# Kernel optimization log

Measured on AMD Instinct MI355X. Metric: run time of the kernel, lower is better.

Reference implementation:

```python
import jax, jax.numpy as jnp
import numpy as np

EMB = 512
N_ROWS = 10000
N_PAIRS = 65536


def setup_inputs() -> dict:
    key = jax.random.key(0)
    ks = jax.random.split(key, 10)
    s1 = 1.0 / np.sqrt(2 * EMB)
    s2 = 1.0 / np.sqrt(128)
    s3 = 1.0 / np.sqrt(64)
    return {
        "pos_pairs": jax.random.randint(ks[0], (N_PAIRS, 3), 0, N_ROWS, dtype=jnp.int32),
        "neg_pairs": jax.random.randint(ks[1], (N_PAIRS, 3), 0, N_ROWS, dtype=jnp.int32),
        "drug_embedding": jax.random.normal(ks[2], (N_ROWS, EMB), dtype=jnp.float32),
        "target_embedding": jax.random.normal(ks[3], (N_ROWS, EMB), dtype=jnp.float32),
        "W1": jax.random.normal(ks[4], (2 * EMB, 128), dtype=jnp.float32) * s1,
        "b1": jnp.zeros((128,), dtype=jnp.float32),
        "W2": jax.random.normal(ks[5], (128, 64), dtype=jnp.float32) * s2,
        "b2": jnp.zeros((64,), dtype=jnp.float32),
        "W3": jax.random.normal(ks[6], (64, 1), dtype=jnp.float32) * s3,
        "b3": jnp.zeros((1,), dtype=jnp.float32),
    }


def _mlp(x, W1, b1, W2, b2, W3, b3):
    h = jax.nn.relu(x @ W1 + b1)
    h = jax.nn.relu(h @ W2 + b2)
    return (h @ W3 + b3)[..., 0]  # [N]


def _pair_loss(pairs, drug_emb, tgt_emb, W1, b1, W2, b2, W3, b3):
    d = drug_emb[pairs[:, 0]]            # [N, EMB]
    t1 = tgt_emb[pairs[:, 1]]            # [N, EMB]
    t2 = tgt_emb[pairs[:, 2]]            # [N, EMB]
    a1 = _mlp(jnp.concatenate([d, t1], axis=-1), W1, b1, W2, b2, W3, b3)
    a2 = _mlp(jnp.concatenate([d, t2], axis=-1), W1, b1, W2, b2, W3, b3)
    # per-pair MSE of scalar affinities = (a1 - a2)^2; mean over pairs
    return jnp.mean((a1 - a2) ** 2)


def reference(pos_pairs, neg_pairs, drug_embedding, target_embedding,
              W1, b1, W2, b2, W3, b3):
    pos = _pair_loss(pos_pairs, drug_embedding, target_embedding, W1, b1, W2, b2, W3, b3)
    neg = _pair_loss(neg_pairs, drug_embedding, target_embedding, W1, b1, W2, b2, W3, b3)
    return pos - neg
```

## Files before the change

kernel.cpp:

```cpp
#include <hip/hip_runtime.h>

#define EMB 512
#define NROWS 10000
#define NPAIRS 65536

typedef __bf16 bf16x8 __attribute__((ext_vector_type(8)));
typedef float  f32x4  __attribute__((ext_vector_type(4)));
typedef unsigned int u32x4 __attribute__((ext_vector_type(4)));

__device__ __forceinline__ void split2(float x0, float x1, unsigned* hw, unsigned* lw) {
    unsigned u0 = __float_as_uint(x0), u1 = __float_as_uint(x1);
    unsigned r0 = u0 + 0x7FFFu + ((u0 >> 16) & 1u);
    unsigned r1 = u1 + 0x7FFFu + ((u1 >> 16) & 1u);
    float h0 = __uint_as_float(r0 & 0xFFFF0000u);
    float h1 = __uint_as_float(r1 & 0xFFFF0000u);
    float l0 = x0 - h0, l1 = x1 - h1;
    unsigned v0 = __float_as_uint(l0), v1 = __float_as_uint(l1);
    unsigned s0 = v0 + 0x7FFFu + ((v0 >> 16) & 1u);
    unsigned s1 = v1 + 0x7FFFu + ((v1 >> 16) & 1u);
    *hw = (r0 >> 16) | (r1 & 0xFFFF0000u);
    *lw = (s0 >> 16) | (s1 & 0xFFFF0000u);
}

__global__ __launch_bounds__(256)
void k0_fragment(const float* __restrict__ W1, const float* __restrict__ W2,
                 unsigned short* __restrict__ W1Fhi, unsigned short* __restrict__ W1Flo,
                 unsigned short* __restrict__ W2Fhi, unsigned short* __restrict__ W2Flo)
{
    int e = blockIdx.x * 256 + threadIdx.x;
    float x;
    unsigned short *hp, *lp;
    if (e < 131072) {
        int i  = e & 7;
        int l  = (e >> 3) & 63;
        int nt = (e >> 9) & 7;
        int kt = (e >> 12) & 15;
        int t  = e >> 16;
        int k = kt * 32 + 8 * (l >> 4) + i;
        int n = nt * 16 + (l & 15);
        x = W1[(t * 512 + k) * 128 + n];
        hp = W1Fhi + e; lp = W1Flo + e;
    } else {
        int e2 = e - 131072;
        int i  = e2 & 7;
        int l  = (e2 >> 3) & 63;
        int nt = (e2 >> 9) & 3;
        int kt = e2 >> 11;
        int k = kt * 32 + 8 * (l >> 4) + i;
        int n = nt * 16 + (l & 15);
        x = W2[k * 64 + n];
        hp = W2Fhi + e2; lp = W2Flo + e2;
    }
    unsigned u = __float_as_uint(x);
    unsigned r = u + 0x7FFFu + ((u >> 16) & 1u);
    float hf = __uint_as_float(r & 0xFFFF0000u);
    float lf = x - hf;
    unsigned v = __float_as_uint(lf);
    unsigned s = v + 0x7FFFu + ((v >> 16) & 1u);
    *hp = (unsigned short)(r >> 16);
    *lp = (unsigned short)(s >> 16);
}

#define K1_TILES 625

__global__ __launch_bounds__(256)
void k1_mfma(const float* __restrict__ drug, const float* __restrict__ tgt,
             const unsigned* __restrict__ W1Fhi, const unsigned* __restrict__ W1Flo,
             const float* __restrict__ b1,
             float* __restrict__ D, float* __restrict__ T)
{
    int bid = blockIdx.x, tid = threadIdx.x;
    bool isT = bid >= K1_TILES;
    int rt = isT ? bid - K1_TILES : bid;
    const float* emb = isT ? tgt : drug;
    float* out = isT ? T : D;
    int row0 = rt * 16;

    int wave = tid >> 6, lane = tid & 63;
    int g = lane >> 4, lm = lane & 15;
    int ntb = wave * 2;

    const u32x4* BH = (const u32x4*)W1Fhi + (isT ? 8192 : 0);
    const u32x4* BL = (const u32x4*)W1Flo + (isT ? 8192 : 0);

    const float* abase = emb + (size_t)(row0 + lm) * EMB + 8 * g;

    f32x4 acc[2];
    #pragma unroll
    for (int j = 0; j < 2; j++) { acc[j][0]=0.f; acc[j][1]=0.f; acc[j][2]=0.f; acc[j][3]=0.f; }

    float4 a0c = *(const float4*)(abase);
    float4 a1c = *(const float4*)(abase + 4);
    u32x4 bh0c = BH[ntb * 64 + lane];
    u32x4 bh1c = BH[(ntb + 1) * 64 + lane];
    u32x4 bl0c = BL[ntb * 64 + lane];
    u32x4 bl1c = BL[(ntb + 1) * 64 + lane];
    __builtin_amdgcn_sched_barrier(0);

    #pragma unroll
    for (int kt = 0; kt < 16; kt++) {
        float4 a0n, a1n;
        u32x4 bh0n, bh1n, bl0n, bl1n;
        if (kt < 15) {
            a0n = *(const float4*)(abase + (kt + 1) * 32);
            a1n = *(const float4*)(abase + (kt + 1) * 32 + 4);
            bh0n = BH[((kt + 1) * 8 + ntb) * 64 + lane];
            bh1n = BH[((kt + 1) * 8 + ntb + 1) * 64 + lane];
            bl0n = BL[((kt + 1) * 8 + ntb) * 64 + lane];
            bl1n = BL[((kt + 1) * 8 + ntb + 1) * 64 + lane];
        }
        __builtin_amdgcn_sched_barrier(0);
        unsigned h0, h1, h2, h3, l0, l1, l2, l3;
        split2(a0c.x, a0c.y, &h0, &l0);
        split2(a0c.z, a0c.w, &h1, &l1);
        split2(a1c.x, a1c.y, &h2, &l2);
        split2(a1c.z, a1c.w, &h3, &l3);
        u32x4 ah, al;
        ah[0]=h0; ah[1]=h1; ah[2]=h2; ah[3]=h3;
        al[0]=l0; al[1]=l1; al[2]=l2; al[3]=l3;
        bf16x8 Ah = __builtin_bit_cast(bf16x8, ah);
        bf16x8 Al = __builtin_bit_cast(bf16x8, al);
        bf16x8 Bh0 = __builtin_bit_cast(bf16x8, bh0c);
        bf16x8 Bh1 = __builtin_bit_cast(bf16x8, bh1c);
        bf16x8 Bl0 = __builtin_bit_cast(bf16x8, bl0c);
        bf16x8 Bl1 = __builtin_bit_cast(bf16x8, bl1c);
        acc[0] = __builtin_amdgcn_mfma_f32_16x16x32_bf16(Ah, Bh0, acc[0], 0, 0, 0);
        acc[1] = __builtin_amdgcn_mfma_f32_16x16x32_bf16(Ah, Bh1, acc[1], 0, 0, 0);
        acc[0] = __builtin_amdgcn_mfma_f32_16x16x32_bf16(Ah, Bl0, acc[0], 0, 0, 0);
        acc[1] = __builtin_amdgcn_mfma_f32_16x16x32_bf16(Ah, Bl1, acc[1], 0, 0, 0);
        acc[0] = __builtin_amdgcn_mfma_f32_16x16x32_bf16(Al, Bh0, acc[0], 0, 0, 0);
        acc[1] = __builtin_amdgcn_mfma_f32_16x16x32_bf16(Al, Bh1, acc[1], 0, 0, 0);
        __builtin_amdgcn_sched_barrier(0);
        a0c = a0n; a1c = a1n;
        bh0c = bh0n; bh1c = bh1n; bl0c = bl0n; bl1c = bl1n;
    }

    #pragma unroll
    for (int j = 0; j < 2; j++) {
        int col = (ntb + j) * 16 + lm;
        float bias = isT ? 0.f : b1[col];
        #pragma unroll
        for (int reg = 0; reg < 4; reg++) {
            int row = row0 + 4 * g + reg;
            out[row * 128 + col] = acc[j][reg] + bias;
        }
    }
}

__global__ __launch_bounds__(256)
void k2_pairs(const float* __restrict__ D, const float* __restrict__ T,
              const int* __restrict__ pos, const int* __restrict__ neg,
              const unsigned* __restrict__ W2Fhi, const unsigned* __restrict__ W2Flo,
              const float* __restrict__ b2, const float* __restrict__ W3,
              double* __restrict__ partials)
{
    __shared__ u32x4 Ash[4][768];

    int tid = threadIdx.x;
    int wave = tid >> 6, lane = tid & 63;
    int g = lane >> 4, lm = lane & 15;
    int rr = lane >> 3, cc = lane & 7;
    int gw = blockIdx.x * 4 + wave;
    const int* pairs = (gw < 2048) ? pos : neg;
    int p0 = (gw & 2047) * 32;

    const float* bp[12];
    #pragma unroll
    for (int it = 0; it < 12; it++) {
        int pr = it * 8 + rr;
        int idxv;
        const float* src;
        if (pr < 32) { idxv = pairs[(p0 + pr) * 3]; src = D; }
        else { int q = pr - 32; idxv = pairs[(p0 + (q >> 1)) * 3 + 1 + (q & 1)]; src = T; }
        bp[it] = src + (size_t)idxv * 128 + ((cc ^ (pr & 7)) << 2);
    }

    u32x4* A4w = &Ash[wave][0];
    const u32x4* BH4 = (const u32x4*)W2Fhi;
    const u32x4* BL4 = (const u32x4*)W2Flo;

    f32x4 acc[4][4];
    #pragma unroll
    for (int mt = 0; mt < 4; mt++)
        #pragma unroll
        for (int nt = 0; nt < 4; nt++) { acc[mt][nt][0]=0.f; acc[mt][nt][1]=0.f; acc[mt][nt][2]=0.f; acc[mt][nt][3]=0.f; }

    #pragma unroll 1
    for (int kt = 0; kt < 4; kt++) {
        u32x4 bh[4], bl[4];
        #pragma unroll
        for (int nt = 0; nt < 4; nt++) {
            bh[nt] = BH4[(kt * 4 + nt) * 64 + lane];
            bl[nt] = BL4[(kt * 4 + nt) * 64 + lane];
        }
        #pragma unroll
        for (int it = 0; it < 12; it++) {
            __builtin_amdgcn_global_load_lds(
                (const __attribute__((address_space(1))) void*)(bp[it] + kt * 32),
                (__attribute__((address_space(3))) void*)((char*)A4w + it * 1024),
                16, 0, 0);
        }
        asm volatile("s_waitcnt vmcnt(0)" ::: "memory");
        #pragma unroll
        for (int mt = 0; mt < 4; mt++) {
            int r = mt * 16 + lm;
            int p = r >> 1;
            int ds = p & 7, ts = r & 7;
            const f32x4* drow = (const f32x4*)(A4w + p * 8);
            const f32x4* trow = (const f32x4*)(A4w + (32 + r) * 8);
            f32x4 d0 = drow[(2 * g) ^ ds];
            f32x4 d1 = drow[(2 * g + 1) ^ ds];
            f32x4 t0 = trow[(2 * g) ^ ts];
            f32x4 t1 = trow[(2 * g + 1) ^ ts];
            float h0 = fmaxf(d0[0] + t0[0], 0.f), h1v = fmaxf(d0[1] + t0[1], 0.f);
            float h2 = fmaxf(d0[2] + t0[2], 0.f), h3 = fmaxf(d0[3] + t0[3], 0.f);
            float h4 = fmaxf(d1[0] + t1[0], 0.f), h5 = fmaxf(d1[1] + t1[1], 0.f);
            float h6 = fmaxf(d1[2] + t1[2], 0.f), h7 = fmaxf(d1[3] + t1[3], 0.f);
            unsigned hq0, hq1, hq2, hq3, lq0, lq1, lq2, lq3;
            split2(h0, h1v, &hq0, &lq0);
            split2(h2, h3,  &hq1, &lq1);
            split2(h4, h5,  &hq2, &lq2);
            split2(h6, h7,  &hq3, &lq3);
            u32x4 ah, al;
            ah[0]=hq0; ah[1]=hq1; ah[2]=hq2; ah[3]=hq3;
            al[0]=lq0; al[1]=lq1; al[2]=lq2; al[3]=lq3;
            bf16x8 Ah = __builtin_bit_cast(bf16x8, ah);
            bf16x8 Al = __builtin_bit_cast(bf16x8, al);
            #pragma unroll
            for (int nt = 0; nt < 4; nt++) {
                bf16x8 Bh = __builtin_bit_cast(bf16x8, bh[nt]);
                bf16x8 Bl = __builtin_bit_cast(bf16x8, bl[nt]);
                acc[mt][nt] = __builtin_amdgcn_mfma_f32_16x16x32_bf16(Ah, Bh, acc[mt][nt], 0, 0, 0);
                acc[mt][nt] = __builtin_amdgcn_mfma_f32_16x16x32_bf16(Ah, Bl, acc[mt][nt], 0, 0, 0);
                acc[mt][nt] = __builtin_amdgcn_mfma_f32_16x16x32_bf16(Al, Bh, acc[mt][nt], 0, 0, 0);
            }
        }
        asm volatile("s_waitcnt lgkmcnt(0)" ::: "memory");
    }

    float b2v[4], w3v[4];
    #pragma unroll
    for (int nt = 0; nt < 4; nt++) { b2v[nt] = b2[nt * 16 + lm]; w3v[nt] = W3[nt * 16 + lm]; }

    float pr[4][4];
    #pragma unroll
    for (int mt = 0; mt < 4; mt++)
        #pragma unroll
        for (int reg = 0; reg < 4; reg++) {
            float s = 0.f;
            #pragma unroll
            for (int nt = 0; nt < 4; nt++) {
                float h2 = fmaxf(acc[mt][nt][reg] + b2v[nt], 0.f);
                s = fmaf(h2, w3v[nt], s);
            }
            pr[mt][reg] = s;
        }
    #pragma unroll
    for (int m = 1; m <= 8; m <<= 1)
        #pragma unroll
        for (int mt = 0; mt < 4; mt++)
            #pragma unroll
            for (int reg = 0; reg < 4; reg++)
                pr[mt][reg] += __shfl_xor(pr[mt][reg], m, 64);

    double dsq = 0.0;
    #pragma unroll
    for (int mt = 0; mt < 4; mt++) {
        float d0 = pr[mt][0] - pr[mt][1];
        float d1 = pr[mt][2] - pr[mt][3];
        dsq += (double)d0 * (double)d0 + (double)d1 * (double)d1;
    }
    dsq += __shfl_xor(dsq, 16, 64);
    dsq += __shfl_xor(dsq, 32, 64);

    __syncthreads();
    if (lane == 0) ((double*)&Ash[wave][0])[0] = dsq;
    __syncthreads();
    if (tid == 0) {
        double sum = 0.0;
        #pragma unroll
        for (int w = 0; w < 4; w++) sum += ((double*)&Ash[w][0])[0];
        partials[blockIdx.x] = sum;
    }
}

__global__ void k3_final(const double* __restrict__ partials, float* __restrict__ out)
{
    int lane = threadIdx.x;
    double sp = 0.0, sn = 0.0;
    #pragma unroll
    for (int i = 0; i < 8; i++) {
        sp += partials[lane + 64 * i];
        sn += partials[512 + lane + 64 * i];
    }
    #pragma unroll
    for (int m = 1; m <= 32; m <<= 1) {
        sp += __shfl_xor(sp, m, 64);
        sn += __shfl_xor(sn, m, 64);
    }
    if (lane == 0) out[0] = (float)((sp - sn) / (double)NPAIRS);
}

extern "C" void kernel_launch(void* const* d_in, const int* in_sizes, int n_in,
                              void* d_out, int out_size, void* d_ws, size_t ws_size,
                              hipStream_t stream) {
    const int*   pos  = (const int*)d_in[0];
    const int*   neg  = (const int*)d_in[1];
    const float* drug = (const float*)d_in[2];
    const float* tgt  = (const float*)d_in[3];
    const float* W1   = (const float*)d_in[4];
    const float* b1   = (const float*)d_in[5];
    const float* W2   = (const float*)d_in[6];
    const float* b2   = (const float*)d_in[7];
    const float* W3   = (const float*)d_in[8];

    float* Dp = (float*)d_ws;
    float* Tp = Dp + NROWS * 128;
    char* base = (char*)(Tp + NROWS * 128);
    unsigned short* W2Fhi = (unsigned short*)base;
    unsigned short* W2Flo = W2Fhi + 8192;
    unsigned short* W1Fhi = W2Flo + 8192;
    unsigned short* W1Flo = W1Fhi + 131072;
    double* partials = (double*)(W1Flo + 131072);
    float* out = (float*)d_out;

    k0_fragment<<<544, 256, 0, stream>>>(W1, W2, W1Fhi, W1Flo, W2Fhi, W2Flo);
    k1_mfma<<<2 * K1_TILES, 256, 0, stream>>>(drug, tgt, (const unsigned*)W1Fhi,
                                              (const unsigned*)W1Flo, b1, Dp, Tp);
    k2_pairs<<<1024, 256, 0, stream>>>(Dp, Tp, pos, neg, (const unsigned*)W2Fhi,
                                       (const unsigned*)W2Flo, b2, W3, partials);
    k3_final<<<1, 64, 0, stream>>>(partials, out);
}
```

Measured before the change: 68.83 us.

## Stage split A-tile in LDS once per block in k1 instead of per-wave recompute

Each block of k1 now loads its 16x512 embedding tile once, splits it into bf16 hi/lo parts, and writes them to XOR-swizzled shared memory. The MFMA loop then reads A fragments from LDS instead of every wave reloading and re-splitting the same rows from global memory. This removes the fourfold redundant global loads and split arithmetic across waves. In exchange it adds 32KB of LDS per block, a barrier, and drops the explicit register prefetch and sched barriers, with launch bounds now requesting 4 blocks per CU.

```diff
diff --git a/kernel.cpp b/kernel.cpp
--- a/kernel.cpp
+++ b/kernel.cpp
@@ -63,12 +63,15 @@
 
 #define K1_TILES 625
 
-__global__ __launch_bounds__(256)
+__global__ __launch_bounds__(256, 4)
 void k1_mfma(const float* __restrict__ drug, const float* __restrict__ tgt,
              const unsigned* __restrict__ W1Fhi, const unsigned* __restrict__ W1Flo,
              const float* __restrict__ b1,
              float* __restrict__ D, float* __restrict__ T)
 {
+    __shared__ unsigned short Ahi[16][512];
+    __shared__ unsigned short Alo[16][512];
+
     int bid = blockIdx.x, tid = threadIdx.x;
     bool isT = bid >= K1_TILES;
     int rt = isT ? bid - K1_TILES : bid;
@@ -80,59 +83,58 @@
     int g = lane >> 4, lm = lane & 15;
     int ntb = wave * 2;
 
+    float4 va[4][2];
+    #pragma unroll
+    for (int i = 0; i < 4; i++) {
+        const float* src = emb + (size_t)(row0 + wave * 4 + i) * EMB + lane * 8;
+        va[i][0] = *(const float4*)src;
+        va[i][1] = *(const float4*)(src + 4);
+    }
+    #pragma unroll
+    for (int i = 0; i < 4; i++) {
+        int row = wave * 4 + i;
+        unsigned h0, h1, h2, h3, l0, l1, l2, l3;
+        split2(va[i][0].x, va[i][0].y, &h0, &l0);
+        split2(va[i][0].z, va[i][0].w, &h1, &l1);
+        split2(va[i][1].x, va[i][1].y, &h2, &l2);
+        split2(va[i][1].z, va[i][1].w, &h3, &l3);
+        u32x4 hq, lq;
+        hq[0]=h0; hq[1]=h1; hq[2]=h2; hq[3]=h3;
+        lq[0]=l0; lq[1]=l1; lq[2]=l2; lq[3]=l3;
+        int c = lane ^ (row & 7);
+        *(u32x4*)((char*)&Ahi[0][0] + row * 1024 + c * 16) = hq;
+        *(u32x4*)((char*)&Alo[0][0] + row * 1024 + c * 16) = lq;
+    }
+    __syncthreads();
+
     const u32x4* BH = (const u32x4*)W1Fhi + (isT ? 8192 : 0);
     const u32x4* BL = (const u32x4*)W1Flo + (isT ? 8192 : 0);
 
-    const float* abase = emb + (size_t)(row0 + lm) * EMB + 8 * g;
-
     f32x4 acc[2];
     #pragma unroll
     for (int j = 0; j < 2; j++) { acc[j][0]=0.f; acc[j][1]=0.f; acc[j][2]=0.f; acc[j][3]=0.f; }
 
-    float4 a0c = *(const float4*)(abase);
-    float4 a1c = *(const float4*)(abase + 4);
-    u32x4 bh0c = BH[ntb * 64 + lane];
-    u32x4 bh1c = BH[(ntb + 1) * 64 + lane];
-    u32x4 bl0c = BL[ntb * 64 + lane];
-    u32x4 bl1c = BL[(ntb + 1) * 64 + lane];
-    __builtin_amdgcn_sched_barrier(0);
-
     #pragma unroll
     for (int kt = 0; kt < 16; kt++) {
-        float4 a0n, a1n;
-        u32x4 bh0n, bh1n, bl0n, bl1n;
-        if (kt < 15) {
-            a0n = *(const float4*)(abase + (kt + 1) * 32);
-            a1n = *(const float4*)(abase + (kt + 1) * 32 + 4);
-            bh0n = BH[((kt + 1) * 8 + ntb) * 64 + lane];
-            bh1n = BH[((kt + 1) * 8 + ntb + 1) * 64 + lane];
-            bl0n = BL[((kt + 1) * 8 + ntb) * 64 + lane];
-            bl1n = BL[((kt + 1) * 8 + ntb + 1) * 64 + lane];
-        }
-        __builtin_amdgcn_sched_barrier(0);
-        unsigned h0, h1, h2, h3, l0, l1, l2, l3;
-        split2(a0c.x, a0c.y, &h0, &l0);
-        split2(a0c.z, a0c.w, &h1, &l1);
-        split2(a1c.x, a1c.y, &h2, &l2);
-        split2(a1c.z, a1c.w, &h3, &l3);
-        u32x4 ah, al;
-        ah[0]=h0; ah[1]=h1; ah[2]=h2; ah[3]=h3;
-        al[0]=l0; al[1]=l1; al[2]=l2; al[3]=l3;
-        bf16x8 Ah = __builtin_bit_cast(bf16x8, ah);
-        bf16x8 Al = __builtin_bit_cast(bf16x8, al);
-        bf16x8 Bh0 = __builtin_bit_cast(bf16x8, bh0c);
-        bf16x8 Bh1 = __builtin_bit_cast(bf16x8, bh1c);
-        bf16x8 Bl0 = __builtin_bit_cast(bf16x8, bl0c);
-        bf16x8 Bl1 = __builtin_bit_cast(bf16x8, bl1c);
+        u32x4 bh0 = BH[(kt * 8 + ntb) * 64 + lane];
+        u32x4 bh1 = BH[(kt * 8 + ntb + 1) * 64 + lane];
+        u32x4 bl0 = BL[(kt * 8 + ntb) * 64 + lane];
+        u32x4 bl1 = BL[(kt * 8 + ntb + 1) * 64 + lane];
+        int c = (kt * 4 + g) ^ (lm & 7);
+        u32x4 ahq = *(const u32x4*)((const char*)&Ahi[0][0] + lm * 1024 + c * 16);
+        u32x4 alq = *(const u32x4*)((const char*)&Alo[0][0] + lm * 1024 + c * 16);
+        bf16x8 Ah = __builtin_bit_cast(bf16x8, ahq);
+        bf16x8 Al = __builtin_bit_cast(bf16x8, alq);
+        bf16x8 Bh0 = __builtin_bit_cast(bf16x8, bh0);
+        bf16x8 Bh1 = __builtin_bit_cast(bf16x8, bh1);
+        bf16x8 Bl0 = __builtin_bit_cast(bf16x8, bl0);
+        bf16x8 Bl1 = __builtin_bit_cast(bf16x8, bl1);
         acc[0] = __builtin_amdgcn_mfma_f32_16x16x32_bf16(Ah, Bh0, acc[0], 0, 0, 0);
         acc[1] = __builtin_amdgcn_mfma_f32_16x16x32_bf16(Ah, Bh1, acc[1], 0, 0, 0);
         acc[0] = __builtin_amdgcn_mfma_f32_16x16x32_bf16(Ah, Bl0, acc[0], 0, 0, 0);
         acc[1] = __builtin_amdgcn_mfma_f32_16x16x32_bf16(Ah, Bl1, acc[1], 0, 0, 0);
         acc[0] = __builtin_amdgcn_mfma_f32_16x16x32_bf16(Al, Bh0, acc[0], 0, 0, 0);
         acc[1] = __builtin_amdgcn_mfma_f32_16x16x32_bf16(Al, Bh1, acc[1], 0, 0, 0);
-        __builtin_amdgcn_sched_barrier(0);
-        a0c = a0n; a1c = a1n;
-        bh0c = bh0n; bh1c = bh1n; bl0c = bl0n; bl1c = bl1n;
     }
 
     #pragma unroll
```

Result: faster. 60.10 us (-12.7%).
